# Kernel optimization log

Hardware: AMD Instinct MI355X
Metric: run time of the kernel (lower is better)

The kernel has to match this reference:

```python
import jax, jax.numpy as jnp
import numpy as np

E = 8        # num_expert
D = 768      # d_model
H = 3072     # expert hidden = 4*d_model
K = 2        # top_k
N = 4096     # tokens
C = 2048


def setup_inputs() -> dict:
    key = jax.random.key(0)
    k0, k1, k2, k3 = jax.random.split(key, 4)
    moe_inp = jax.random.normal(k0, (N, D), dtype=jnp.float32)
    gate_w = jax.random.normal(k1, (D, E), dtype=jnp.float32) / np.sqrt(D).astype(np.float32)
    gate_b = jnp.zeros((E,), dtype=jnp.float32)
    w1 = jax.random.normal(k2, (E, D, H), dtype=jnp.float32) / np.sqrt(D).astype(np.float32)
    b1 = jnp.zeros((E, H), dtype=jnp.float32)
    w2 = jax.random.normal(k3, (E, H, D), dtype=jnp.float32) / np.sqrt(H).astype(np.float32)
    b2 = jnp.zeros((E, D), dtype=jnp.float32)
    return {"moe_inp": moe_inp, "gate_w": gate_w, "gate_b": gate_b,
            "w1": w1, "b1": b1, "w2": w2, "b2": b2}


def reference(moe_inp, gate_w, gate_b, w1, b1, w2, b2):
    # --- NaiveGate: linear scores, top-k experts, softmax over the k scores ---
    logits = moe_inp @ gate_w + gate_b                      # [N, E]
    top_v, top_i = jax.lax.top_k(logits, K)                 # [N, K]
    gate_score = jax.nn.softmax(top_v, axis=-1)             # [N, K]

    # --- scatter tokens to expert-contiguous capacity buffers (MOEScatter) ---
    flat_e = top_i.reshape(-1)                              # [N*K] expert id per slot
    onehot = jax.nn.one_hot(flat_e, E, dtype=jnp.int32)     # [N*K, E]
    # running position of each token inside its expert's buffer
    pos = jnp.sum(jnp.cumsum(onehot, axis=0) * onehot, axis=1) - 1  # [N*K]
    x_rep = jnp.repeat(moe_inp, K, axis=0)                  # [N*K, D]
    xe = jnp.zeros((E, C, D), dtype=moe_inp.dtype).at[flat_e, pos].set(x_rep, mode='drop')

    # --- grouped expert FFN (expert_fn): per-expert batched GEMMs ---
    h = jax.nn.gelu(jnp.einsum('ecd,edh->ech', xe, w1) + b1[:, None, :])
    ye = jnp.einsum('ech,ehd->ecd', h, w2) + b2[:, None, :]  # [E, C, D]

    # --- gather back to token order (MOEGather) and combine with gate scores ---
    y_flat = ye.at[flat_e, pos].get(mode='fill', fill_value=0.0)  # [N*K, D]
    out = jnp.einsum('nkd,nk->nd', y_flat.reshape(N, K, D), gate_score)
    return out
```

## Files before the change

### kernel.cpp

```cpp
#include <hip/hip_runtime.h>
#include <hip/hip_bf16.h>
#include <math.h>

#define NT    4096
#define DM    768
#define HD    3072
#define NE    8
#define CAP   2048
#define SLOTS_MAX 9216

typedef __attribute__((ext_vector_type(8))) short bf16x8;
typedef __attribute__((ext_vector_type(4))) float f32x4;

__device__ __forceinline__ unsigned short f2bf(float f) {
  unsigned int u = __float_as_uint(f);
  unsigned int r = (u + 0x7fffu + ((u >> 16) & 1u)) >> 16;
  return (unsigned short)r;
}

__device__ __forceinline__ void async16(const unsigned short* g, unsigned short* l) {
  __builtin_amdgcn_global_load_lds((const __attribute__((address_space(1))) void*)g,
                                   (__attribute__((address_space(3))) void*)l,
                                   16, 0, 0);
}

__global__ void convert_x_kernel(const float* __restrict__ x,
                                 unsigned short* __restrict__ xb) {
  int i = (blockIdx.x * 256 + threadIdx.x) * 4;
  float4 v = *(const float4*)(x + i);
  uint2 o;
  o.x = (unsigned int)f2bf(v.x) | ((unsigned int)f2bf(v.y) << 16);
  o.y = (unsigned int)f2bf(v.z) | ((unsigned int)f2bf(v.w) << 16);
  *(uint2*)(xb + i) = o;
}

__global__ void transpose_kernel(const float* __restrict__ src,
                                 unsigned short* __restrict__ dst,
                                 int R, int src_stride, int col_off,
                                 size_t src_e_stride, size_t dst_e_stride) {
  __shared__ unsigned short tile[64][34];
  const float* s = src + blockIdx.z * src_e_stride;
  unsigned short* d = dst + blockIdx.z * dst_e_stride;
  const int r0 = blockIdx.y * 32;
  const int c0 = blockIdx.x * 64;
  const int t = threadIdx.x;
#pragma unroll
  for (int i = 0; i < 4; i++) {
    int row = (t >> 5) + i * 8;
    int cu  = t & 31;
    const float2 v = *(const float2*)(s + (size_t)(r0 + row) * src_stride + col_off + c0 + cu * 2);
    tile[cu * 2][row]     = f2bf(v.x);
    tile[cu * 2 + 1][row] = f2bf(v.y);
  }
  __syncthreads();
#pragma unroll
  for (int i = 0; i < 4; i++) {
    int drow = (t >> 4) + i * 16;
    int ru   = t & 15;
    unsigned int v = *(const unsigned int*)&tile[drow][ru * 2];
    *(unsigned int*)(d + (size_t)(c0 + drow) * R + r0 + ru * 2) = v;
  }
}

__global__ void gate_dots_kernel(const float* __restrict__ inp,
                                 const float* __restrict__ gw,
                                 const float* __restrict__ gb,
                                 int2* __restrict__ tope,
                                 float2* __restrict__ tops) {
  const int tok  = blockIdx.x * 4 + (threadIdx.x >> 6);
  const int lane = threadIdx.x & 63;
  const float* x = inp + (size_t)tok * DM;
  float acc[NE];
#pragma unroll
  for (int e = 0; e < NE; e++) acc[e] = 0.f;
  for (int d = lane; d < DM; d += 64) {
    float xv = x[d];
    const float4 w0 = *(const float4*)(gw + d * NE);
    const float4 w1v = *(const float4*)(gw + d * NE + 4);
    acc[0] += xv * w0.x; acc[1] += xv * w0.y;
    acc[2] += xv * w0.z; acc[3] += xv * w0.w;
    acc[4] += xv * w1v.x; acc[5] += xv * w1v.y;
    acc[6] += xv * w1v.z; acc[7] += xv * w1v.w;
  }
#pragma unroll
  for (int e = 0; e < NE; e++) {
    float v = acc[e];
#pragma unroll
    for (int m = 32; m > 0; m >>= 1) v += __shfl_xor(v, m, 64);
    acc[e] = v + gb[e];
  }
  if (lane == 0) {
    float bv = -1e30f, sv = -1e30f; int bi = 0, si = 0;
#pragma unroll
    for (int e = 0; e < NE; e++) {
      float v = acc[e];
      if (v > bv)      { sv = bv; si = bi; bv = v; bi = e; }
      else if (v > sv) { sv = v;  si = e; }
    }
    float e1 = expf(sv - bv);
    float s0 = 1.f / (1.f + e1);
    float s1 = e1 / (1.f + e1);
    tope[tok] = make_int2(bi, si);
    tops[tok] = make_float2(s0, s1);
  }
}

__device__ __forceinline__ int agg_inc(int* lcnt, int key) {
  const int lane = threadIdx.x & 63;
  int p = 0;
#pragma unroll
  for (int ee = 0; ee < NE; ee++) {
    unsigned long long m = __ballot(key == ee);
    if (m) {
      int leader = __ffsll(m) - 1;
      int n = __popcll(m);
      int b = 0;
      if (lane == leader) b = atomicAdd(&lcnt[ee], n);
      b = __shfl(b, leader, 64);
      if (key == ee) p = b + __popcll(m & ((1ull << lane) - 1ull));
    }
  }
  return p;
}

__global__ void assign_kernel(const int2* __restrict__ tope,
                              int* __restrict__ cnt,
                              int* __restrict__ base,
                              int* __restrict__ src,
                              int2* __restrict__ pos) {
  __shared__ int lcnt[NE];
  const int t = threadIdx.x;
  if (t < NE) lcnt[t] = 0;
  __syncthreads();
  for (int i = t; i < NT; i += 1024) {
    int2 e = tope[i];
    int p0 = agg_inc(lcnt, e.x);
    int p1 = agg_inc(lcnt, e.y);
    if (p0 < CAP) src[e.x * CAP + p0] = i;
    if (p1 < CAP) src[e.y * CAP + p1] = i;
    pos[i] = make_int2(p0, p1);
  }
  __syncthreads();
  if (t == 0) {
    int b = 0;
    for (int e = 0; e < NE; e++) {
      int c = min(lcnt[e], CAP);
      cnt[e] = c;
      base[e] = b;
      b += (c + 127) & ~127;
    }
  }
}

__global__ __launch_bounds__(256) void gemm1_kernel(
    const unsigned short* __restrict__ xb,
    const unsigned short* __restrict__ w1t,
    const float* __restrict__ b1,
    const int* __restrict__ cnt,
    const int* __restrict__ base,
    const int* __restrict__ src,
    unsigned short* __restrict__ h,
    int hoff, int chunk) {
  const int b = blockIdx.x;
  const int e = b & 7;
  const int idx = b >> 3;
  const int m0 = (idx & 15) * 128;
  const int n0 = (idx >> 4) * 128;
  const int count = cnt[e];
  if (m0 >= count) return;
  const int hb = base[e];

  __shared__ unsigned short As[128 * 32];
  __shared__ unsigned short Bs[128 * 32];

  const int t = threadIdx.x;
  const int lane = t & 63;
  const int wave = t >> 6;
  const int r0 = t >> 2;
  const int kc = (t & 3) * 8;

  const int tok0 = (m0 + r0      < count) ? src[e * CAP + m0 + r0]      : 0;
  const int tok1 = (m0 + r0 + 64 < count) ? src[e * CAP + m0 + r0 + 64] : 0;
  const unsigned short* aptr0 = xb + (size_t)tok0 * DM + kc;
  const unsigned short* aptr1 = xb + (size_t)tok1 * DM + kc;
  const unsigned short* w1e = w1t + (size_t)e * chunk * DM;
  const unsigned short* bptr0 = w1e + (size_t)(n0 + r0) * DM + kc;
  const unsigned short* bptr1 = bptr0 + (size_t)64 * DM;

  unsigned short* as0 = As + (wave * 64) * 8;
  unsigned short* as1 = As + (256 + wave * 64) * 8;
  unsigned short* bs0 = Bs + (wave * 64) * 8;
  unsigned short* bs1 = Bs + (256 + wave * 64) * 8;

  const int wrow = (wave >> 1) * 64;
  const int wcol = (wave & 1) * 64;
  const int lrow = lane & 15;
  const int koff = (lane >> 4) * 8;

  f32x4 acc[4][4];
#pragma unroll
  for (int i = 0; i < 4; i++)
#pragma unroll
    for (int j = 0; j < 4; j++) acc[i][j] = (f32x4){0.f, 0.f, 0.f, 0.f};

  for (int k0 = 0; k0 < DM; k0 += 32) {
    async16(aptr0 + k0, as0);
    async16(aptr1 + k0, as1);
    async16(bptr0 + k0, bs0);
    async16(bptr1 + k0, bs1);
    __syncthreads();
    bf16x8 af[4], bfr[4];
#pragma unroll
    for (int i = 0; i < 4; i++)
      af[i] = *(const bf16x8*)(As + (wrow + i * 16 + lrow) * 32 + koff);
#pragma unroll
    for (int j = 0; j < 4; j++)
      bfr[j] = *(const bf16x8*)(Bs + (wcol + j * 16 + lrow) * 32 + koff);
#pragma unroll
    for (int i = 0; i < 4; i++)
#pragma unroll
      for (int j = 0; j < 4; j++)
        acc[i][j] = __builtin_amdgcn_mfma_f32_16x16x32_bf16(af[i], bfr[j], acc[i][j], 0, 0, 0);
    __syncthreads();
  }

  const int q4 = (lane >> 4) * 4;
  const int c = lane & 15;
  unsigned short* hrow = h + (size_t)(hb + m0) * chunk + n0;
#pragma unroll
  for (int j = 0; j < 4; j++) {
    const float bias = b1[e * HD + hoff + n0 + wcol + j * 16 + c];
#pragma unroll
    for (int i = 0; i < 4; i++) {
#pragma unroll
      for (int r = 0; r < 4; r++) {
        int m = wrow + i * 16 + q4 + r;
        float v = acc[i][j][r] + bias;
        float u2 = 1.5957691216f * (v + 0.044715f * v * v * v);
        float g = v / (1.f + __expf(-u2));
        hrow[(size_t)m * chunk + wcol + j * 16 + c] = f2bf(g);
      }
    }
  }
}

__global__ __launch_bounds__(256) void gemm2_kernel(
    const unsigned short* __restrict__ h,
    const unsigned short* __restrict__ w2t,
    const int* __restrict__ cnt,
    const int* __restrict__ base,
    float* __restrict__ ye,
    int chunk, int add_prev) {
  const int b = blockIdx.x;
  const int e = b & 7;
  const int kh = (b >> 3) & 1;
  const int idx = b >> 4;
  const int m0 = (idx & 15) * 128;
  const int n0 = (idx >> 4) * 128;
  const int count = cnt[e];
  if (m0 >= count) return;
  const int hb = base[e];
  const int khalf = chunk >> 1;

  __shared__ unsigned short As[128 * 32];
  __shared__ unsigned short Bs[128 * 32];

  const int t = threadIdx.x;
  const int lane = t & 63;
  const int wave = t >> 6;
  const int r0 = t >> 2;
  const int kc = (t & 3) * 8;

  const unsigned short* aptr0 = h + (size_t)(hb + m0 + r0) * chunk + kh * khalf + kc;
  const unsigned short* aptr1 = aptr0 + (size_t)64 * chunk;
  const unsigned short* w2e = w2t + (size_t)e * DM * chunk;
  const unsigned short* bptr0 = w2e + (size_t)(n0 + r0) * chunk + kh * khalf + kc;
  const unsigned short* bptr1 = bptr0 + (size_t)64 * chunk;

  unsigned short* as0 = As + (wave * 64) * 8;
  unsigned short* as1 = As + (256 + wave * 64) * 8;
  unsigned short* bs0 = Bs + (wave * 64) * 8;
  unsigned short* bs1 = Bs + (256 + wave * 64) * 8;

  const int wrow = (wave >> 1) * 64;
  const int wcol = (wave & 1) * 64;
  const int lrow = lane & 15;
  const int koff = (lane >> 4) * 8;

  f32x4 acc[4][4];
#pragma unroll
  for (int i = 0; i < 4; i++)
#pragma unroll
    for (int j = 0; j < 4; j++) acc[i][j] = (f32x4){0.f, 0.f, 0.f, 0.f};

  for (int k0 = 0; k0 < khalf; k0 += 32) {
    async16(aptr0 + k0, as0);
    async16(aptr1 + k0, as1);
    async16(bptr0 + k0, bs0);
    async16(bptr1 + k0, bs1);
    __syncthreads();
    bf16x8 af[4], bfr[4];
#pragma unroll
    for (int i = 0; i < 4; i++)
      af[i] = *(const bf16x8*)(As + (wrow + i * 16 + lrow) * 32 + koff);
#pragma unroll
    for (int j = 0; j < 4; j++)
      bfr[j] = *(const bf16x8*)(Bs + (wcol + j * 16 + lrow) * 32 + koff);
#pragma unroll
    for (int i = 0; i < 4; i++)
#pragma unroll
      for (int j = 0; j < 4; j++)
        acc[i][j] = __builtin_amdgcn_mfma_f32_16x16x32_bf16(af[i], bfr[j], acc[i][j], 0, 0, 0);
    __syncthreads();
  }

  const int q4 = (lane >> 4) * 4;
  const int c = lane & 15;
  float* yrow = ye + (size_t)kh * SLOTS_MAX * DM + (size_t)(hb + m0) * DM + n0;
#pragma unroll
  for (int i = 0; i < 4; i++) {
#pragma unroll
    for (int r = 0; r < 4; r++) {
      int m = wrow + i * 16 + q4 + r;
#pragma unroll
      for (int j = 0; j < 4; j++) {
        int n = wcol + j * 16 + c;
        float v = acc[i][j][r];
        if (add_prev) v += yrow[(size_t)m * DM + n];
        yrow[(size_t)m * DM + n] = v;
      }
    }
  }
}

__global__ void gather_kernel(const float* __restrict__ ye,
                              const float* __restrict__ b2,
                              const int2* __restrict__ tope,
                              const float2* __restrict__ tops,
                              const int2* __restrict__ pos,
                              const int* __restrict__ base,
                              float* __restrict__ out) {
  int idx = blockIdx.x * 256 + threadIdx.x;
  int tok = idx / (DM / 4);
  int d4 = (idx % (DM / 4)) * 4;
  int2 e = tope[tok];
  float2 s = tops[tok];
  int2 p = pos[tok];
  const float* ye1 = ye + (size_t)SLOTS_MAX * DM;
  float4 r = make_float4(0.f, 0.f, 0.f, 0.f);
  if (p.x < CAP) {
    size_t row = (size_t)(base[e.x] + p.x) * DM + d4;
    const float4 va = *(const float4*)(ye + row);
    const float4 vb = *(const float4*)(ye1 + row);
    const float4 bb = *(const float4*)(b2 + e.x * DM + d4);
    r.x += s.x * (va.x + vb.x + bb.x); r.y += s.x * (va.y + vb.y + bb.y);
    r.z += s.x * (va.z + vb.z + bb.z); r.w += s.x * (va.w + vb.w + bb.w);
  }
  if (p.y < CAP) {
    size_t row = (size_t)(base[e.y] + p.y) * DM + d4;
    const float4 va = *(const float4*)(ye + row);
    const float4 vb = *(const float4*)(ye1 + row);
    const float4 bb = *(const float4*)(b2 + e.y * DM + d4);
    r.x += s.y * (va.x + vb.x + bb.x); r.y += s.y * (va.y + vb.y + bb.y);
    r.z += s.y * (va.z + vb.z + bb.z); r.w += s.y * (va.w + vb.w + bb.w);
  }
  *(float4*)(out + (size_t)tok * DM + d4) = r;
}

extern "C" void kernel_launch(void* const* d_in, const int* in_sizes, int n_in,
                              void* d_out, int out_size, void* d_ws, size_t ws_size,
                              hipStream_t stream) {
  const float* inp = (const float*)d_in[0];
  const float* gw  = (const float*)d_in[1];
  const float* gb  = (const float*)d_in[2];
  const float* w1  = (const float*)d_in[3];
  const float* b1  = (const float*)d_in[4];
  const float* w2  = (const float*)d_in[5];
  const float* b2  = (const float*)d_in[6];
  float* out = (float*)d_out;

  const size_t meta = 164352;
  const int cands[8] = {3072, 1536, 1024, 768, 512, 384, 256, 128};
  int chunk = 128;
  for (int ci = 0; ci < 8; ci++) {
    int c = cands[ci];
    size_t need = meta + (size_t)NT * DM * 2
                + (size_t)NE * c * DM * 2
                + (size_t)SLOTS_MAX * c * 2
                + 2 * (size_t)SLOTS_MAX * DM * 4;
    if (need <= ws_size) { chunk = c; break; }
  }

  char* ws = (char*)d_ws;
  int*    cnt  = (int*)(ws);
  int*    base = (int*)(ws + 256);
  int*    srcb = (int*)(ws + 512);
  int2*   tope = (int2*)(ws + 66048);
  float2* tops = (float2*)(ws + 98816);
  int2*   pos  = (int2*)(ws + 131584);
  size_t off = meta;
  unsigned short* xb = (unsigned short*)(ws + off);  off += (size_t)NT * DM * 2;
  unsigned short* wt = (unsigned short*)(ws + off);  off += (size_t)NE * chunk * DM * 2;
  unsigned short* hc = (unsigned short*)(ws + off);  off += (size_t)SLOTS_MAX * chunk * 2;
  float* ye = (float*)(ws + off);

  convert_x_kernel<<<(NT * DM) / 1024, 256, 0, stream>>>(inp, xb);
  gate_dots_kernel<<<NT / 4, 256, 0, stream>>>(inp, gw, gb, tope, tops);
  assign_kernel<<<1, 1024, 0, stream>>>(tope, cnt, base, srcb, pos);

  for (int c = 0; c < HD; c += chunk) {
    transpose_kernel<<<dim3(chunk / 64, DM / 32, NE), 256, 0, stream>>>(
        w1, wt, DM, HD, c, (size_t)DM * HD, (size_t)chunk * DM);
    gemm1_kernel<<<NE * 16 * (chunk / 128), 256, 0, stream>>>(
        xb, wt, b1, cnt, base, srcb, hc, c, chunk);
    transpose_kernel<<<dim3(DM / 64, chunk / 32, NE), 256, 0, stream>>>(
        w2 + (size_t)c * DM, wt, chunk, DM, 0, (size_t)HD * DM, (size_t)DM * chunk);
    gemm2_kernel<<<NE * 2 * 16 * (DM / 128), 256, 0, stream>>>(
        hc, wt, cnt, base, ye, chunk, c == 0 ? 0 : 1);
  }

  gather_kernel<<<(NT * DM / 4) / 256, 256, 0, stream>>>(ye, b2, tope, tops, pos, base, out);
}
```

Before: 382.7 us.

## Double-buffer LDS tiles in both expert GEMM kernels to overlap loads with MFMA

Both grouped GEMM kernels now use two LDS buffers for the A and B tiles. The next K-slice's async global-to-LDS loads are issued before computing on the current buffer, and one barrier per iteration is removed. The goal is to hide global load latency behind MFMA work. In exchange, LDS use per block doubles to 32 KB, which may lower occupancy. The compiler may also insert a vmcnt wait before the LDS reads, which would serialize the prefetch and cancel the overlap.

```diff
diff --git a/kernel.cpp b/kernel.cpp
--- a/kernel.cpp
+++ b/kernel.cpp
@@ -170,8 +170,8 @@
   if (m0 >= count) return;
   const int hb = base[e];
 
-  __shared__ unsigned short As[128 * 32];
-  __shared__ unsigned short Bs[128 * 32];
+  __shared__ unsigned short As[2][128 * 32];
+  __shared__ unsigned short Bs[2][128 * 32];
 
   const int t = threadIdx.x;
   const int lane = t & 63;
@@ -187,11 +187,6 @@
   const unsigned short* bptr0 = w1e + (size_t)(n0 + r0) * DM + kc;
   const unsigned short* bptr1 = bptr0 + (size_t)64 * DM;
 
-  unsigned short* as0 = As + (wave * 64) * 8;
-  unsigned short* as1 = As + (256 + wave * 64) * 8;
-  unsigned short* bs0 = Bs + (wave * 64) * 8;
-  unsigned short* bs1 = Bs + (256 + wave * 64) * 8;
-
   const int wrow = (wave >> 1) * 64;
   const int wcol = (wave & 1) * 64;
   const int lrow = lane & 15;
@@ -203,26 +198,43 @@
 #pragma unroll
     for (int j = 0; j < 4; j++) acc[i][j] = (f32x4){0.f, 0.f, 0.f, 0.f};
 
-  for (int k0 = 0; k0 < DM; k0 += 32) {
-    async16(aptr0 + k0, as0);
-    async16(aptr1 + k0, as1);
-    async16(bptr0 + k0, bs0);
-    async16(bptr1 + k0, bs1);
+#define STAGE1(bi, kk) do {                                   \
+    unsigned short* A_ = As[bi] + wave * 512;                 \
+    unsigned short* B_ = Bs[bi] + wave * 512;                 \
+    async16(aptr0 + (kk), A_);                                \
+    async16(aptr1 + (kk), A_ + 2048);                         \
+    async16(bptr0 + (kk), B_);                                \
+    async16(bptr1 + (kk), B_ + 2048);                         \
+  } while (0)
+
+#define COMPUTE1(bi) do {                                               \
+    const unsigned short* A_ = As[bi];                                  \
+    const unsigned short* B_ = Bs[bi];                                  \
+    bf16x8 af[4], bfr[4];                                               \
+    _Pragma("unroll")                                                   \
+    for (int i = 0; i < 4; i++)                                         \
+      af[i] = *(const bf16x8*)(A_ + (wrow + i * 16 + lrow) * 32 + koff);\
+    _Pragma("unroll")                                                   \
+    for (int j = 0; j < 4; j++)                                         \
+      bfr[j] = *(const bf16x8*)(B_ + (wcol + j * 16 + lrow) * 32 + koff);\
+    _Pragma("unroll")                                                   \
+    for (int i = 0; i < 4; i++)                                         \
+      _Pragma("unroll")                                                 \
+      for (int j = 0; j < 4; j++)                                       \
+        acc[i][j] = __builtin_amdgcn_mfma_f32_16x16x32_bf16(af[i], bfr[j], acc[i][j], 0, 0, 0); \
+  } while (0)
+
+  const int NS = DM / 32;
+  STAGE1(0, 0);
+  __syncthreads();
+  int buf = 0;
+  for (int ts = 0; ts < NS - 1; ++ts) {
+    STAGE1(buf ^ 1, (ts + 1) * 32);
+    COMPUTE1(buf);
     __syncthreads();
-    bf16x8 af[4], bfr[4];
-#pragma unroll
-    for (int i = 0; i < 4; i++)
-      af[i] = *(const bf16x8*)(As + (wrow + i * 16 + lrow) * 32 + koff);
-#pragma unroll
-    for (int j = 0; j < 4; j++)
-      bfr[j] = *(const bf16x8*)(Bs + (wcol + j * 16 + lrow) * 32 + koff);
-#pragma unroll
-    for (int i = 0; i < 4; i++)
-#pragma unroll
-      for (int j = 0; j < 4; j++)
-        acc[i][j] = __builtin_amdgcn_mfma_f32_16x16x32_bf16(af[i], bfr[j], acc[i][j], 0, 0, 0);
-    __syncthreads();
-  }
+    buf ^= 1;
+  }
+  COMPUTE1(buf);
 
   const int q4 = (lane >> 4) * 4;
   const int c = lane & 15;
@@ -242,6 +254,8 @@
       }
     }
   }
+#undef STAGE1
+#undef COMPUTE1
 }
 
 __global__ __launch_bounds__(256) void gemm2_kernel(
@@ -262,8 +276,8 @@
   const int hb = base[e];
   const int khalf = chunk >> 1;
 
-  __shared__ unsigned short As[128 * 32];
-  __shared__ unsigned short Bs[128 * 32];
+  __shared__ unsigned short As[2][128 * 32];
+  __shared__ unsigned short Bs[2][128 * 32];
 
   const int t = threadIdx.x;
   const int lane = t & 63;
@@ -277,11 +291,6 @@
   const unsigned short* bptr0 = w2e + (size_t)(n0 + r0) * chunk + kh * khalf + kc;
   const unsigned short* bptr1 = bptr0 + (size_t)64 * chunk;
 
-  unsigned short* as0 = As + (wave * 64) * 8;
-  unsigned short* as1 = As + (256 + wave * 64) * 8;
-  unsigned short* bs0 = Bs + (wave * 64) * 8;
-  unsigned short* bs1 = Bs + (256 + wave * 64) * 8;
-
   const int wrow = (wave >> 1) * 64;
   const int wcol = (wave & 1) * 64;
   const int lrow = lane & 15;
@@ -293,26 +302,43 @@
 #pragma unroll
     for (int j = 0; j < 4; j++) acc[i][j] = (f32x4){0.f, 0.f, 0.f, 0.f};
 
-  for (int k0 = 0; k0 < khalf; k0 += 32) {
-    async16(aptr0 + k0, as0);
-    async16(aptr1 + k0, as1);
-    async16(bptr0 + k0, bs0);
-    async16(bptr1 + k0, bs1);
+#define STAGE2(bi, kk) do {                                   \
+    unsigned short* A_ = As[bi] + wave * 512;                 \
+    unsigned short* B_ = Bs[bi] + wave * 512;                 \
+    async16(aptr0 + (kk), A_);                                \
+    async16(aptr1 + (kk), A_ + 2048);                         \
+    async16(bptr0 + (kk), B_);                                \
+    async16(bptr1 + (kk), B_ + 2048);                         \
+  } while (0)
+
+#define COMPUTE2(bi) do {                                               \
+    const unsigned short* A_ = As[bi];                                  \
+    const unsigned short* B_ = Bs[bi];                                  \
+    bf16x8 af[4], bfr[4];                                               \
+    _Pragma("unroll")                                                   \
+    for (int i = 0; i < 4; i++)                                         \
+      af[i] = *(const bf16x8*)(A_ + (wrow + i * 16 + lrow) * 32 + koff);\
+    _Pragma("unroll")                                                   \
+    for (int j = 0; j < 4; j++)                                         \
+      bfr[j] = *(const bf16x8*)(B_ + (wcol + j * 16 + lrow) * 32 + koff);\
+    _Pragma("unroll")                                                   \
+    for (int i = 0; i < 4; i++)                                         \
+      _Pragma("unroll")                                                 \
+      for (int j = 0; j < 4; j++)                                       \
+        acc[i][j] = __builtin_amdgcn_mfma_f32_16x16x32_bf16(af[i], bfr[j], acc[i][j], 0, 0, 0); \
+  } while (0)
+
+  const int NS = khalf >> 5;
+  STAGE2(0, 0);
+  __syncthreads();
+  int buf = 0;
+  for (int ts = 0; ts < NS - 1; ++ts) {
+    STAGE2(buf ^ 1, (ts + 1) * 32);
+    COMPUTE2(buf);
     __syncthreads();
-    bf16x8 af[4], bfr[4];
-#pragma unroll
-    for (int i = 0; i < 4; i++)
-      af[i] = *(const bf16x8*)(As + (wrow + i * 16 + lrow) * 32 + koff);
-#pragma unroll
-    for (int j = 0; j < 4; j++)
-      bfr[j] = *(const bf16x8*)(Bs + (wcol + j * 16 + lrow) * 32 + koff);
-#pragma unroll
-    for (int i = 0; i < 4; i++)
-#pragma unroll
-      for (int j = 0; j < 4; j++)
-        acc[i][j] = __builtin_amdgcn_mfma_f32_16x16x32_bf16(af[i], bfr[j], acc[i][j], 0, 0, 0);
-    __syncthreads();
-  }
+    buf ^= 1;
+  }
+  COMPUTE2(buf);
 
   const int q4 = (lane >> 4) * 4;
   const int c = lane & 15;
@@ -331,6 +357,8 @@
       }
     }
   }
+#undef STAGE2
+#undef COMPUTE2
 }
 
 __global__ void gather_kernel(const float* __restrict__ ye,
```

New measurement: 377.2 us. About the same (-1.4%).
